# Kernel optimization log

Measured on AMD Instinct MI355X. Metric: run time of the kernel, lower is better.

Reference implementation:

```python
import jax, jax.numpy as jnp
import numpy as np

N_NODES = 20000
N_EDGES = 160000
N_GRAPHS = 100
IN_CH = 64
EDGE_DIM = 8
NEG_SLOPE = 0.2


def _gatv2(x, edge_index, edge_attr, Wl, Wr, We, att, b, heads, ch, n_nodes):
    # GATv2Conv: e_ij = att . leaky_relu(Wl x_j + Wr x_i [+ We e_ij]), softmax over dst i,
    # out_i = sum_j alpha_ij * (Wl x_j), concat heads, + bias.
    src, dst = edge_index[0], edge_index[1]
    xl = (x @ Wl).reshape(-1, heads, ch)  # [N,H,C] source-side transform
    xr = (x @ Wr).reshape(-1, heads, ch)  # [N,H,C] target-side transform
    m = xl[src] + xr[dst]                 # [E,H,C]
    if edge_attr is not None:
        m = m + (edge_attr @ We).reshape(-1, heads, ch)
    m = jax.nn.leaky_relu(m, NEG_SLOPE)
    logit = jnp.einsum('ehc,hc->eh', m, att)                     # [E,H]
    mx = jax.ops.segment_max(logit, dst, num_segments=n_nodes)   # [N,H]
    ex = jnp.exp(logit - mx[dst])
    den = jax.ops.segment_sum(ex, dst, num_segments=n_nodes)     # [N,H]
    alpha = ex / (den[dst] + 1e-16)                              # [E,H]
    out = jax.ops.segment_sum(alpha[:, :, None] * xl[src], dst, num_segments=n_nodes)
    return out.reshape(-1, heads * ch) + b


def setup_inputs() -> dict:
    key = jax.random.key(0)
    ks = jax.random.split(key, 24)
    def rn(k, shape, fan_in):
        return jax.random.normal(k, shape, dtype=jnp.float32) / np.sqrt(fan_in)
    inp = {}
    inp['x'] = jax.random.normal(ks[0], (N_NODES, IN_CH), dtype=jnp.float32)
    inp['edge_attr'] = jax.random.uniform(ks[1], (N_EDGES, EDGE_DIM), dtype=jnp.float32)
    inp['Wl1'] = rn(ks[2], (IN_CH, 1024), IN_CH)
    inp['Wr1'] = rn(ks[3], (IN_CH, 1024), IN_CH)
    inp['We1'] = rn(ks[4], (EDGE_DIM, 1024), EDGE_DIM)
    inp['att1'] = rn(ks[5], (4, 256), 256)
    inp['b1'] = jnp.zeros((1024,), jnp.float32)
    inp['Wl2'] = rn(ks[6], (1024, 256), 1024)
    inp['Wr2'] = rn(ks[7], (1024, 256), 1024)
    inp['We2'] = rn(ks[8], (EDGE_DIM, 256), EDGE_DIM)
    inp['att2'] = rn(ks[9], (4, 64), 64)
    inp['b2'] = jnp.zeros((256,), jnp.float32)
    inp['Wlp'] = rn(ks[10], (256, 384), 256)
    inp['Wrp'] = rn(ks[11], (256, 384), 256)
    inp['attp'] = rn(ks[12], (6, 64), 64)
    inp['bp'] = jnp.zeros((384,), jnp.float32)
    inp['Wfc1'] = rn(ks[13], (384, 64), 384)
    inp['bfc1'] = jnp.zeros((64,), jnp.float32)
    inp['Wfc2'] = rn(ks[14], (64, 1), 64)
    inp['bfc2'] = jnp.zeros((1,), jnp.float32)
    inp['edge_index'] = jax.random.randint(ks[15], (2, N_EDGES), 0, N_NODES, dtype=jnp.int32)
    inp['edge_index_master'] = jax.random.randint(ks[16], (2, N_EDGES), 0, N_NODES, dtype=jnp.int32)
    inp['n_nodes'] = jnp.full((N_GRAPHS,), N_NODES // N_GRAPHS, dtype=jnp.int32)
    return inp


def reference(x, edge_attr, Wl1, Wr1, We1, att1, b1, Wl2, Wr2, We2, att2, b2,
              Wlp, Wrp, attp, bp, Wfc1, bfc1, Wfc2, bfc2,
              edge_index, edge_index_master, n_nodes):
    h = _gatv2(x, edge_index, edge_attr, Wl1, Wr1, We1, att1, b1, 4, 256, N_NODES)
    h = jax.nn.relu(h)
    h = _gatv2(h, edge_index, edge_attr, Wl2, Wr2, We2, att2, b2, 4, 64, N_NODES)
    h = jax.nn.relu(h)
    h = _gatv2(h, edge_index_master, None, Wlp, Wrp, None, attp, bp, 6, 64, N_NODES)
    last_idx = jnp.cumsum(n_nodes) - 1          # master node = last node of each graph
    master = h[last_idx]                        # [G,384] (dropout p=0 -> identity)
    z = jax.nn.relu(master @ Wfc1 + bfc1)
    return z @ Wfc2 + bfc2                      # [G,1]
```

## Files before the change

### kernel.cpp

```cpp
#include <hip/hip_runtime.h>
#include <hip/hip_bf16.h>

#define DIV_UP(a,b) (((a)+(b)-1)/(b))

typedef __attribute__((ext_vector_type(8))) short short8;
typedef __attribute__((ext_vector_type(4))) float floatx4;
typedef _Float16 half2t __attribute__((ext_vector_type(2)));

static __device__ __forceinline__ unsigned short f2bf(float v) {
    unsigned u = __builtin_bit_cast(unsigned, v);
    u += 0x7fffu + ((u >> 16) & 1u);
    return (unsigned short)(u >> 16);
}
static __device__ __forceinline__ unsigned short f2h(float v) {
    _Float16 h = (_Float16)v;
    return __builtin_bit_cast(unsigned short, h);
}
static __device__ __forceinline__ float fexp2(float x) { return __builtin_amdgcn_exp2f(x); }

static __device__ __forceinline__ half2t mk_h2(float lo, float hi) {
    half2t h; h[0] = (_Float16)lo; h[1] = (_Float16)hi; return h;
}
static __device__ __forceinline__ unsigned ph2(float lo, float hi) {
    return __builtin_bit_cast(unsigned, mk_h2(lo, hi));
}
static __device__ __forceinline__ float fdot2h(half2t a, half2t b, float c) {
    return __builtin_amdgcn_fdot2(a, b, c, false);
}
static __device__ __forceinline__ unsigned uget(const uint4 v, int k) {
    return k == 0 ? v.x : k == 1 ? v.y : k == 2 ? v.z : v.w;
}
static __device__ __forceinline__ float h2lo(half2t h) { return (float)h[0]; }
static __device__ __forceinline__ float h2hi(half2t h) { return (float)h[1]; }

template <int CPL> struct RawT;
template <> struct RawT<8> { using T = uint4; };
template <> struct RawT<4> { using T = uint2; };
template <> struct RawT<2> { using T = unsigned; };

template <int CPL>
static __device__ __forceinline__ void loadh2(const unsigned short* p, half2t* d) {
    if constexpr (CPL == 8) {
        uint4 v = *(const uint4*)p;
        d[0] = __builtin_bit_cast(half2t, v.x);
        d[1] = __builtin_bit_cast(half2t, v.y);
        d[2] = __builtin_bit_cast(half2t, v.z);
        d[3] = __builtin_bit_cast(half2t, v.w);
    } else if constexpr (CPL == 4) {
        uint2 v = *(const uint2*)p;
        d[0] = __builtin_bit_cast(half2t, v.x);
        d[1] = __builtin_bit_cast(half2t, v.y);
    } else {
        unsigned v = *(const unsigned*)p;
        d[0] = __builtin_bit_cast(half2t, v);
    }
}

template <int CPL>
static __device__ __forceinline__ void store_bf16v(unsigned short* p, const float* s) {
    unsigned short tmp[CPL];
#pragma unroll
    for (int c = 0; c < CPL; ++c) tmp[c] = f2bf(s[c]);
    if constexpr (CPL == 8) *(uint4*)p = *(uint4*)tmp;
    else if constexpr (CPL == 4) *(ushort4*)p = *(ushort4*)tmp;
    else if constexpr (CPL == 2) *(ushort2*)p = *(ushort2*)tmp;
    else p[0] = tmp[0];
}

template <int CTRL>
static __device__ __forceinline__ float dpp_mv(float x) {
    int r = __builtin_amdgcn_update_dpp(0, __builtin_bit_cast(int, x), CTRL, 0xF, 0xF, false);
    return __builtin_bit_cast(float, r);
}
template <int G>
static __device__ __forceinline__ float group_reduce(float x) {
    x += dpp_mv<0xB1>(x);
    x += dpp_mv<0x4E>(x);
    x += dpp_mv<0x124>(x);
    x += dpp_mv<0x128>(x);
    if constexpr (G >= 32) x += __shfl_xor(x, 16, 64);
    if constexpr (G >= 64) x += __shfl_xor(x, 32, 64);
    return x;
}

static __device__ __forceinline__ void tr_pair(const float* Wa, const float* Wb, int K, int Nn,
                                               unsigned short* Wt, int i) {
    int tot = K * Nn;
    const float* W = (i < tot) ? Wa : Wb;
    unsigned short* dst = Wt + ((i < tot) ? 0 : (size_t)Nn * K);
    int ii = (i < tot) ? i : i - tot;
    int k = ii % K, n = ii / K;
    dst[(size_t)n * K + k] = f2bf(W[(size_t)k * Nn + n]);
}

__global__ void prep_all(const float* __restrict__ x,
                         const float* __restrict__ Wl1, const float* __restrict__ Wr1,
                         const float* __restrict__ Wl2, const float* __restrict__ Wr2,
                         const float* __restrict__ Wlp, const float* __restrict__ Wrp,
                         unsigned short* __restrict__ xbf,
                         unsigned short* __restrict__ wt1, unsigned short* __restrict__ wt2,
                         unsigned short* __restrict__ wt3, int N) {
    const int S1 = 2 * 64 * 1024, S2 = 2 * 1024 * 256, S3 = 2 * 256 * 384;
    int id = blockIdx.x * blockDim.x + threadIdx.x;
    if (id < S1) tr_pair(Wl1, Wr1, 64, 1024, wt1, id);
    else if (id < S1 + S2) tr_pair(Wl2, Wr2, 1024, 256, wt2, id - S1);
    else if (id < S1 + S2 + S3) tr_pair(Wlp, Wrp, 256, 384, wt3, id - S1 - S2);
    else {
        int i = id - S1 - S2 - S3;
        if (i < N * 64) xbf[i] = f2bf(x[i]);
    }
}

#define GLOAD_LDS16(gp, lp) \
    __builtin_amdgcn_global_load_lds((const __attribute__((address_space(1))) void*)(gp), \
                                     (__attribute__((address_space(3))) void*)(lp), 16, 0, 0)

__global__ __launch_bounds__(256) void gemm_mfma(
    const unsigned short* __restrict__ A, const unsigned short* __restrict__ Bt,
    unsigned short* __restrict__ CL, unsigned short* __restrict__ CR,
    int M, int NL, int K) {
    __shared__ unsigned short As[128 * 32];
    __shared__ unsigned short Bs[128 * 32];
    const int tid = threadIdx.x;
    const int m0 = blockIdx.y * 128, n0 = blockIdx.x * 128;
    const bool left = (n0 < NL);
    unsigned short* Cb = left ? CL : CR;
    const int nbase = left ? n0 : n0 - NL;
    const int wave = tid >> 6, lane = tid & 63;
    const int wm = (wave >> 1) * 64, wn = (wave & 1) * 64;
    const int r15 = lane & 15, quad = lane >> 4;
    const int srow = lane >> 2, scol = (lane & 3) * 8;
    const int arow0 = m0 + 32 * wave + srow;
    const int brow0 = n0 + 32 * wave + srow;
    const unsigned short* ap0 = A + (size_t)arow0 * K + scol;
    const unsigned short* ap1 = ap0 + (size_t)16 * K;
    const unsigned short* bp0 = Bt + (size_t)brow0 * K + scol;
    const unsigned short* bp1 = bp0 + (size_t)16 * K;
    unsigned short* alds0 = As + (32 * wave) * 32;
    unsigned short* alds1 = alds0 + 16 * 32;
    unsigned short* blds0 = Bs + (32 * wave) * 32;
    unsigned short* blds1 = blds0 + 16 * 32;
    const bool av0 = arow0 < M, av1 = (arow0 + 16) < M;
    floatx4 acc[4][4];
#pragma unroll
    for (int i = 0; i < 4; ++i)
#pragma unroll
        for (int j = 0; j < 4; ++j) acc[i][j] = (floatx4)0.f;

    for (int k0 = 0; k0 < K; k0 += 32) {
        if (av0) GLOAD_LDS16(ap0, alds0);
        if (av1) GLOAD_LDS16(ap1, alds1);
        GLOAD_LDS16(bp0, blds0);
        GLOAD_LDS16(bp1, blds1);
        ap0 += 32; ap1 += 32; bp0 += 32; bp1 += 32;
        __syncthreads();
        short8 af[4], bfr[4];
#pragma unroll
        for (int i = 0; i < 4; ++i)
            af[i] = *(const short8*)(&As[(wm + i * 16 + r15) * 32 + quad * 8]);
#pragma unroll
        for (int j = 0; j < 4; ++j)
            bfr[j] = *(const short8*)(&Bs[(wn + j * 16 + r15) * 32 + quad * 8]);
#pragma unroll
        for (int i = 0; i < 4; ++i)
#pragma unroll
            for (int j = 0; j < 4; ++j)
                acc[i][j] = __builtin_amdgcn_mfma_f32_16x16x32_bf16(af[i], bfr[j], acc[i][j], 0, 0, 0);
        __syncthreads();
    }
#pragma unroll
    for (int i = 0; i < 4; ++i)
#pragma unroll
        for (int j = 0; j < 4; ++j)
#pragma unroll
            for (int r = 0; r < 4; ++r) {
                int m = m0 + wm + i * 16 + quad * 4 + r;
                int n = nbase + wn + j * 16 + r15;
                if (m < M) Cb[(size_t)m * NL + n] = f2h(acc[i][j][r]);
            }
}

__global__ void count2_kernel(const int* __restrict__ dst0, const int* __restrict__ dst1,
                              int E, int N, int* __restrict__ cnt) {
    int e = blockIdx.x * blockDim.x + threadIdx.x;
    if (e < E) atomicAdd(&cnt[dst0[e]], 1);
    else if (e < 2 * E) atomicAdd(&cnt[N + dst1[e - E]], 1);
}

__global__ __launch_bounds__(1024) void scan_kernel(const int* __restrict__ cnt_all, int N,
                                                    int* __restrict__ off_all, int* __restrict__ cur_all) {
    const int* cnt = cnt_all + blockIdx.x * N;
    int* off = off_all + blockIdx.x * (N + 1);
    int* cur = cur_all + blockIdx.x * N;
    __shared__ int part[1024];
    int t = threadIdx.x;
    int per = (N + 1023) >> 10;
    int base = t * per;
    int s = 0;
    for (int i = 0; i < per; ++i) { int idx = base + i; if (idx < N) s += cnt[idx]; }
    part[t] = s;
    __syncthreads();
    for (int d2 = 1; d2 < 1024; d2 <<= 1) {
        int v = (t >= d2) ? part[t - d2] : 0;
        __syncthreads();
        part[t] += v;
        __syncthreads();
    }
    int pre = (t == 0) ? 0 : part[t - 1];
    for (int i = 0; i < per; ++i) {
        int idx = base + i;
        if (idx < N) { off[idx] = pre; cur[idx] = pre; pre += cnt[idx]; }
    }
    if (t == 1023) off[N] = part[1023];
}

__global__ void fill2_kernel(const int* __restrict__ src0, const int* __restrict__ dst0,
                             const int* __restrict__ src1, const int* __restrict__ dst1,
                             int E, int N, int* __restrict__ cur, int2* __restrict__ edges,
                             int* __restrict__ srcs) {
    int e = blockIdx.x * blockDim.x + threadIdx.x;
    if (e < E) {
        int p = atomicAdd(&cur[dst0[e]], 1);
        edges[p] = make_int2(src0[e], e);
        srcs[p] = src0[e];
    } else if (e < 2 * E) {
        int i = e - E;
        int p = atomicAdd(&cur[N + dst1[i]], 1);
        srcs[E + p] = src1[i];
    }
}

__global__ void ea_gather_kernel(const float* __restrict__ ea, const int2* __restrict__ edges,
                                 uint4* __restrict__ ead, int E) {
    int j = blockIdx.x * blockDim.x + threadIdx.x;
    if (j >= E) return;
    int ey = edges[j].y;
    const float4* s = (const float4*)(ea + (size_t)ey * 8);
    float4 a = s[0], b = s[1];
    uint4 o0, o1;
    o0.x = ph2(a.x, a.x); o0.y = ph2(a.y, a.y);
    o0.z = ph2(a.z, a.z); o0.w = ph2(a.w, a.w);
    o1.x = ph2(b.x, b.x); o1.y = ph2(b.y, b.y);
    o1.z = ph2(b.z, b.z); o1.w = ph2(b.w, b.w);
    ead[2 * j]     = o0;
    ead[2 * j + 1] = o1;
}

template <int D, int CPL, int G, int NE>
static __device__ __forceinline__ void hase_group(
    const unsigned short* __restrict__ xl, const uint4* __restrict__ ej,
    const int* __restrict__ sj, const unsigned* wbu,
    const half2t (&att2)[CPL / 2], const half2t (&xr2)[CPL / 2], int c0,
    float& m, float& l, float (&acc)[CPL]) {
    constexpr int P = CPL / 2;
    int src[NE];
#pragma unroll
    for (int n = 0; n < NE; ++n) src[n] = sj[n];
    uint4 ev0[NE], ev1[NE];
#pragma unroll
    for (int n = 0; n < NE; ++n) { ev0[n] = ej[2 * n]; ev1[n] = ej[2 * n + 1]; }
    half2t xv[NE][P], z[NE][P];
#pragma unroll
    for (int n = 0; n < NE; ++n) {
        loadh2<CPL>(xl + (size_t)src[n] * D + c0, xv[n]);
#pragma unroll
        for (int p = 0; p < P; ++p) z[n][p] = xv[n][p] + xr2[p];
    }
#pragma unroll
    for (int k = 0; k < 8; ++k) {
        half2t wk[P];
        if constexpr (CPL == 8) {
            uint4 w4 = *(const uint4*)(wbu + k * (D / 2));
            wk[0] = __builtin_bit_cast(half2t, w4.x);
            wk[1] = __builtin_bit_cast(half2t, w4.y);
            wk[2] = __builtin_bit_cast(half2t, w4.z);
            wk[3] = __builtin_bit_cast(half2t, w4.w);
        } else {
            uint2 w2 = *(const uint2*)(wbu + k * (D / 2));
            wk[0] = __builtin_bit_cast(half2t, w2.x);
            wk[1] = __builtin_bit_cast(half2t, w2.y);
        }
#pragma unroll
        for (int n = 0; n < NE; ++n) {
            unsigned eu = (k < 4) ? uget(ev0[n], k) : uget(ev1[n], k - 4);
            half2t e2 = __builtin_bit_cast(half2t, eu);
#pragma unroll
            for (int p = 0; p < P; ++p)
                z[n][p] = __builtin_elementwise_fma(e2, wk[p], z[n][p]);
        }
    }
    const half2t c02 = mk_h2(0.2f, 0.2f);
    float lg[NE];
#pragma unroll
    for (int n = 0; n < NE; ++n) {
        float t = 0.f;
#pragma unroll
        for (int p = 0; p < P; ++p) {
            half2t zz = z[n][p];
            half2t lz = __builtin_elementwise_max(zz, zz * c02);
            t = fdot2h(att2[p], lz, t);
        }
        lg[n] = group_reduce<G>(t);
    }
    float mn = m;
#pragma unroll
    for (int n = 0; n < NE; ++n) mn = fmaxf(mn, lg[n]);
    float sc = fexp2(m - mn);
    float pr[NE], ps = 0.f;
#pragma unroll
    for (int n = 0; n < NE; ++n) { pr[n] = fexp2(lg[n] - mn); ps += pr[n]; }
    m = mn;
    l = fmaf(l, sc, ps);
#pragma unroll
    for (int p = 0; p < P; ++p) {
        float t0 = pr[0] * h2lo(xv[0][p]);
        float t1 = pr[0] * h2hi(xv[0][p]);
#pragma unroll
        for (int n = 1; n < NE; ++n) {
            t0 = fmaf(pr[n], h2lo(xv[n][p]), t0);
            t1 = fmaf(pr[n], h2hi(xv[n][p]), t1);
        }
        acc[2 * p]     = fmaf(acc[2 * p],     sc, t0);
        acc[2 * p + 1] = fmaf(acc[2 * p + 1], sc, t1);
    }
}

template <int D, int C, int CB, int WPN, bool RELU>
__global__ __launch_bounds__(256) void attn_hase(
    const unsigned short* __restrict__ xl, const unsigned short* __restrict__ xr,
    const uint4* __restrict__ ead4,
    const float* __restrict__ We, const float* __restrict__ att,
    const int* __restrict__ srcs, const int* __restrict__ off,
    const float* __restrict__ bias, unsigned short* __restrict__ outp, int N) {
    constexpr int CPL = CB / 64;
    constexpr int P = CPL / 2;
    constexpr int HW = CB / C;
    constexpr int G = 64 / HW;
    constexpr int NPB = 4 / WPN;
    __shared__ unsigned wsh[4 * D];
    for (int idx = threadIdx.x; idx < 4 * D; idx += 256) {
        int k = idx / (D / 2);
        int r = idx - k * (D / 2);
        int c = 2 * r;
        wsh[idx] = ph2(We[(size_t)k * D + c], We[(size_t)k * D + c + 1]);
    }
    __syncthreads();

    const int wid = threadIdx.x >> 6, lane = threadIdx.x & 63;
    const int wv = wid % WPN, wn = wid / WPN;
    const int c0 = wv * CB + lane * CPL;
    const unsigned* wbu = wsh + wv * (CB / 2) + lane * (CPL / 2);

    const float L2E = 1.4426950408889634f;
    half2t att2[P];
#pragma unroll
    for (int p = 0; p < P; ++p)
        att2[p] = mk_h2(att[c0 + 2 * p] * L2E, att[c0 + 2 * p + 1] * L2E);

    for (int node = blockIdx.x * NPB + wn; node < N; node += gridDim.x * NPB) {
        half2t xr2[P];
        loadh2<CPL>(xr + (size_t)node * D + c0, xr2);
        float m = -1e30f, l = 0.f, acc[CPL];
#pragma unroll
        for (int c = 0; c < CPL; ++c) acc[c] = 0.f;

        const int jb = __builtin_amdgcn_readfirstlane(off[node]);
        const int je = __builtin_amdgcn_readfirstlane(off[node + 1]);
        int j = jb;
        for (; j + 4 <= je; j += 4)
            hase_group<D, CPL, G, 4>(xl, ead4 + 2 * j, srcs + j, wbu, att2, xr2, c0, m, l, acc);
        for (; j < je; ++j)
            hase_group<D, CPL, G, 1>(xl, ead4 + 2 * j, srcs + j, wbu, att2, xr2, c0, m, l, acc);

        float inv = 1.f / (l + 1e-16f);
        float r[CPL];
#pragma unroll
        for (int c = 0; c < CPL; ++c) {
            r[c] = fmaf(acc[c], inv, bias[c0 + c]);
            if constexpr (RELU) r[c] = fmaxf(r[c], 0.f);
        }
        store_bf16v<CPL>(outp + (size_t)node * D + c0, r);
    }
}

template <int D, int CPL, int G, int NE>
static __device__ __forceinline__ void noe_group(
    const unsigned short* __restrict__ xl, const int* __restrict__ sj,
    const half2t (&att2)[CPL / 2], const half2t (&xr2)[CPL / 2], int c0,
    float& m, float& l, float (&acc)[CPL]) {
    constexpr int P = CPL / 2;
    int src[NE];
#pragma unroll
    for (int n = 0; n < NE; ++n) src[n] = sj[n];
    half2t xv[NE][P];
#pragma unroll
    for (int n = 0; n < NE; ++n)
        loadh2<CPL>(xl + (size_t)src[n] * D + c0, xv[n]);
    const half2t c02 = mk_h2(0.2f, 0.2f);
    float lg[NE];
#pragma unroll
    for (int n = 0; n < NE; ++n) {
        float t = 0.f;
#pragma unroll
        for (int p = 0; p < P; ++p) {
            half2t zz = xv[n][p] + xr2[p];
            half2t lz = __builtin_elementwise_max(zz, zz * c02);
            t = fdot2h(att2[p], lz, t);
        }
        lg[n] = group_reduce<G>(t);
    }
    float mn = m;
#pragma unroll
    for (int n = 0; n < NE; ++n) mn = fmaxf(mn, lg[n]);
    float sc = fexp2(m - mn);
    float pr[NE], ps = 0.f;
#pragma unroll
    for (int n = 0; n < NE; ++n) { pr[n] = fexp2(lg[n] - mn); ps += pr[n]; }
    m = mn;
    l = fmaf(l, sc, ps);
#pragma unroll
    for (int p = 0; p < P; ++p) {
        float t0 = pr[0] * h2lo(xv[0][p]);
        float t1 = pr[0] * h2hi(xv[0][p]);
#pragma unroll
        for (int n = 1; n < NE; ++n) {
            t0 = fmaf(pr[n], h2lo(xv[n][p]), t0);
            t1 = fmaf(pr[n], h2hi(xv[n][p]), t1);
        }
        acc[2 * p]     = fmaf(acc[2 * p],     sc, t0);
        acc[2 * p + 1] = fmaf(acc[2 * p + 1], sc, t1);
    }
}

template <int D, int C, int CB, bool RELU>
static __device__ __forceinline__ void attn_wave3(
    const unsigned short* __restrict__ xl, const unsigned short* __restrict__ xr,
    const float* __restrict__ att,
    const int* __restrict__ srcs, int jb, int je,
    const float* __restrict__ bias, float* __restrict__ outp,
    int node, int cb, int lane) {
    constexpr int CPL = CB / 64;
    constexpr int P = CPL / 2;
    constexpr int HW = CB / C;
    constexpr int G = 64 / HW;
    const int c0 = cb + lane * CPL;
    const float L2E = 1.4426950408889634f;

    half2t xr2[P], att2[P];
    loadh2<CPL>(xr + (size_t)node * D + c0, xr2);
#pragma unroll
    for (int p = 0; p < P; ++p)
        att2[p] = mk_h2(att[c0 + 2 * p] * L2E, att[c0 + 2 * p + 1] * L2E);

    float m = -1e30f, l = 0.f, acc[CPL];
#pragma unroll
    for (int c = 0; c < CPL; ++c) acc[c] = 0.f;

    int j = jb;
    for (; j + 4 <= je; j += 4)
        noe_group<D, CPL, G, 4>(xl, srcs + j, att2, xr2, c0, m, l, acc);
    for (; j < je; ++j)
        noe_group<D, CPL, G, 1>(xl, srcs + j, att2, xr2, c0, m, l, acc);

    float inv = 1.f / (l + 1e-16f);
    float* out = outp + (size_t)node * D + c0;
    float tmp[CPL];
#pragma unroll
    for (int c = 0; c < CPL; ++c) {
        float r = fmaf(acc[c], inv, bias[c0 + c]);
        if constexpr (RELU) r = fmaxf(r, 0.f);
        tmp[c] = r;
    }
    if constexpr (CPL == 4) *(float4*)out = *(float4*)tmp;
    else if constexpr (CPL == 2) *(float2*)out = *(float2*)tmp;
    else out[0] = tmp[0];
}

template <int D, int C, int CB0, int CB1, bool RELU>
__global__ __launch_bounds__(256) void attn_noe(
    const unsigned short* __restrict__ xl, const unsigned short* __restrict__ xr,
    const float* __restrict__ att,
    const int* __restrict__ srcs, const int* __restrict__ off,
    const float* __restrict__ bias, float* __restrict__ outp, int N) {
    const int wid = threadIdx.x >> 6, lane = threadIdx.x & 63;
    const int gw = blockIdx.x * 4 + wid;
    const int node = gw >> 1, wv = gw & 1;
    if (node >= N) return;
    const int jb = __builtin_amdgcn_readfirstlane(off[node]);
    const int je = __builtin_amdgcn_readfirstlane(off[node + 1]);
    if (wv == 0)
        attn_wave3<D, C, CB0, RELU>(xl, xr, att, srcs, jb, je, bias, outp, node, 0, lane);
    else
        attn_wave3<D, C, CB1, RELU>(xl, xr, att, srcs, jb, je, bias, outp, node, CB0, lane);
}

__global__ void mlp_kernel(const float* __restrict__ h3, const int* __restrict__ nn,
                           const float* __restrict__ Wfc1, const float* __restrict__ bfc1,
                           const float* __restrict__ Wfc2, const float* __restrict__ bfc2,
                           float* __restrict__ out, int G) {
    int g = blockIdx.x, t = threadIdx.x;
    int s = 0;
    for (int k = 0; k <= g; ++k) s += nn[k];
    const float* row = h3 + (size_t)(s - 1) * 384;
    float z = bfc1[t];
    for (int k = 0; k < 384; ++k) z = fmaf(row[k], Wfc1[k * 64 + t], z);
    z = fmaxf(z, 0.f);
    float v = z * Wfc2[t];
#pragma unroll
    for (int o = 32; o; o >>= 1) v += __shfl_xor(v, o, 64);
    if (t == 0) out[g] = v + bfc2[0];
}

extern "C" void kernel_launch(void* const* d_in, const int* in_sizes, int n_in,
                              void* d_out, int out_size, void* d_ws, size_t ws_size,
                              hipStream_t stream) {
    const float* x    = (const float*)d_in[0];
    const float* ea   = (const float*)d_in[1];
    const float* Wl1  = (const float*)d_in[2];
    const float* Wr1  = (const float*)d_in[3];
    const float* We1  = (const float*)d_in[4];
    const float* att1 = (const float*)d_in[5];
    const float* b1   = (const float*)d_in[6];
    const float* Wl2  = (const float*)d_in[7];
    const float* Wr2  = (const float*)d_in[8];
    const float* We2  = (const float*)d_in[9];
    const float* att2 = (const float*)d_in[10];
    const float* b2   = (const float*)d_in[11];
    const float* Wlp  = (const float*)d_in[12];
    const float* Wrp  = (const float*)d_in[13];
    const float* attp = (const float*)d_in[14];
    const float* bp   = (const float*)d_in[15];
    const float* Wfc1 = (const float*)d_in[16];
    const float* bfc1 = (const float*)d_in[17];
    const float* Wfc2 = (const float*)d_in[18];
    const float* bfc2 = (const float*)d_in[19];
    const int* ei     = (const int*)d_in[20];
    const int* eim    = (const int*)d_in[21];
    const int* nn     = (const int*)d_in[22];

    const int N = in_sizes[0] / 64;
    const int E = in_sizes[20] / 2;
    const int G = in_sizes[22];
    const int* src1 = ei,  *dst1 = ei + E;
    const int* srcm = eim, *dstm = eim + E;

    char* w = (char*)d_ws;
    size_t o = 0;
    auto alloc = [&](size_t b) { size_t r = o; o += (b + 255) & ~(size_t)255; return r; };
    char* R1 = w + alloc((size_t)N * 2048 * 2);
    unsigned short* xl1 = (unsigned short*)R1;
    unsigned short* xr1 = xl1 + (size_t)N * 1024;
    unsigned short* xl3 = (unsigned short*)R1;
    unsigned short* xr3 = xl3 + (size_t)N * 384;
    float* h3 = (float*)(R1 + (size_t)N * 768 * 2 + 256);
    unsigned short* h1   = (unsigned short*)(w + alloc((size_t)N * 1024 * 2));
    char* R2 = w + alloc((size_t)N * 512 * 2);
    unsigned short* xl2 = (unsigned short*)R2;
    unsigned short* xr2 = xl2 + (size_t)N * 256;
    unsigned short* h2   = (unsigned short*)(w + alloc((size_t)N * 256 * 2));
    unsigned short* xbf  = (unsigned short*)(w + alloc((size_t)N * 64 * 2));
    unsigned short* wt1  = (unsigned short*)(w + alloc((size_t)2048 * 64 * 2));
    unsigned short* wt2  = (unsigned short*)(w + alloc((size_t)512 * 1024 * 2));
    unsigned short* wt3  = (unsigned short*)(w + alloc((size_t)768 * 256 * 2));
    int*  cnt   = (int*)(w + alloc((size_t)2 * N * 4));
    int*  off   = (int*)(w + alloc((size_t)2 * (N + 1) * 4));
    int*  cur   = (int*)(w + alloc((size_t)2 * N * 4));
    char* eReg  = w + alloc((size_t)2 * E * 8 + 4096);
    int2* edges = (int2*)eReg;
    int*  srcs  = (int*)(eReg + (size_t)E * 8);
    (void)ws_size; (void)n_in; (void)out_size;

    uint4* ead1 = (uint4*)R2;
    uint4* ead2 = (uint4*)h1;

    dim3 blk(256);

    {
        int tot = 2 * 64 * 1024 + 2 * 1024 * 256 + 2 * 256 * 384 + N * 64;
        prep_all<<<DIV_UP(tot, 256), blk, 0, stream>>>(x, Wl1, Wr1, Wl2, Wr2, Wlp, Wrp,
                                                       xbf, wt1, wt2, wt3, N);
    }

    hipMemsetAsync(cnt, 0, (size_t)2 * N * 4, stream);
    count2_kernel<<<DIV_UP(2 * E, 256), blk, 0, stream>>>(dst1, dstm, E, N, cnt);
    scan_kernel<<<2, 1024, 0, stream>>>(cnt, N, off, cur);
    fill2_kernel<<<DIV_UP(2 * E, 256), blk, 0, stream>>>(src1, dst1, srcm, dstm, E, N, cur,
                                                         edges, srcs);
    ea_gather_kernel<<<DIV_UP(E, 256), blk, 0, stream>>>(ea, edges, ead1, E);
    const int* off3 = off + (N + 1);
    const int* srcs3 = srcs + E;

    gemm_mfma<<<dim3(2048 / 128, DIV_UP(N, 128)), blk, 0, stream>>>(
        xbf, wt1, xl1, xr1, N, 1024, 64);
    attn_hase<1024, 256, 512, 2, true><<<2560, blk, 0, stream>>>(
        xl1, xr1, ead1, We1, att1, srcs, off, b1, h1, N);

    gemm_mfma<<<dim3(512 / 128, DIV_UP(N, 128)), blk, 0, stream>>>(
        h1, wt2, xl2, xr2, N, 256, 1024);
    ea_gather_kernel<<<DIV_UP(E, 256), blk, 0, stream>>>(ea, edges, ead2, E);
    attn_hase<256, 64, 256, 1, true><<<1280, blk, 0, stream>>>(
        xl2, xr2, ead2, We2, att2, srcs, off, b2, h2, N);

    gemm_mfma<<<dim3(768 / 128, DIV_UP(N, 128)), blk, 0, stream>>>(
        h2, wt3, xl3, xr3, N, 384, 256);
    attn_noe<384, 64, 256, 128, false><<<DIV_UP(N, 2), blk, 0, stream>>>(
        xl3, xr3, attp, srcs3, off3, bp, h3, N);

    mlp_kernel<<<G, 64, 0, stream>>>(h3, nn, Wfc1, bfc1, Wfc2, bfc2, (float*)d_out, G);
}
```

Before: 420.5 us.

## Split each node's edge list across two waves and merge softmax partials via LDS

The edge-attention kernel now assigns two waves per node feature slice. Each wave processes half of the node's incoming edges with an online softmax, and the partial max, sum and accumulators are merged through shared memory before the output is written. This doubles parallelism per node to hide gather latency on xl. In exchange it adds LDS traffic, two block-wide barriers per iteration, and fewer nodes per block.

```diff
diff --git a/kernel.cpp b/kernel.cpp
--- a/kernel.cpp
+++ b/kernel.cpp
@@ -336,8 +336,10 @@
     constexpr int P = CPL / 2;
     constexpr int HW = CB / C;
     constexpr int G = 64 / HW;
-    constexpr int NPB = 4 / WPN;
+    constexpr int NW = WPN * 2;
+    constexpr int NPB = 4 / NW;
     __shared__ unsigned wsh[4 * D];
+    __shared__ float cmb[NPB][WPN][64][CPL + 2];
     for (int idx = threadIdx.x; idx < 4 * D; idx += 256) {
         int k = idx / (D / 2);
         int r = idx - k * (D / 2);
@@ -347,7 +349,10 @@
     __syncthreads();
 
     const int wid = threadIdx.x >> 6, lane = threadIdx.x & 63;
-    const int wv = wid % WPN, wn = wid / WPN;
+    const int wn = wid / NW;
+    const int wr = wid - wn * NW;
+    const int wv = wr % WPN;
+    const int ep = wr / WPN;
     const int c0 = wv * CB + lane * CPL;
     const unsigned* wbu = wsh + wv * (CB / 2) + lane * (CPL / 2);
 
@@ -357,29 +362,51 @@
     for (int p = 0; p < P; ++p)
         att2[p] = mk_h2(att[c0 + 2 * p] * L2E, att[c0 + 2 * p + 1] * L2E);
 
-    for (int node = blockIdx.x * NPB + wn; node < N; node += gridDim.x * NPB) {
+    for (int base = blockIdx.x * NPB; base < N; base += gridDim.x * NPB) {
+        const int node = base + wn;
+        float m = -1e30f, l = 0.f, acc[CPL];
+#pragma unroll
+        for (int c = 0; c < CPL; ++c) acc[c] = 0.f;
         half2t xr2[P];
-        loadh2<CPL>(xr + (size_t)node * D + c0, xr2);
-        float m = -1e30f, l = 0.f, acc[CPL];
-#pragma unroll
-        for (int c = 0; c < CPL; ++c) acc[c] = 0.f;
-
-        const int jb = __builtin_amdgcn_readfirstlane(off[node]);
-        const int je = __builtin_amdgcn_readfirstlane(off[node + 1]);
-        int j = jb;
-        for (; j + 4 <= je; j += 4)
-            hase_group<D, CPL, G, 4>(xl, ead4 + 2 * j, srcs + j, wbu, att2, xr2, c0, m, l, acc);
-        for (; j < je; ++j)
-            hase_group<D, CPL, G, 1>(xl, ead4 + 2 * j, srcs + j, wbu, att2, xr2, c0, m, l, acc);
-
-        float inv = 1.f / (l + 1e-16f);
-        float r[CPL];
-#pragma unroll
-        for (int c = 0; c < CPL; ++c) {
-            r[c] = fmaf(acc[c], inv, bias[c0 + c]);
-            if constexpr (RELU) r[c] = fmaxf(r[c], 0.f);
-        }
-        store_bf16v<CPL>(outp + (size_t)node * D + c0, r);
+#pragma unroll
+        for (int p = 0; p < P; ++p) xr2[p] = mk_h2(0.f, 0.f);
+
+        if (node < N) {
+            loadh2<CPL>(xr + (size_t)node * D + c0, xr2);
+            const int jb = __builtin_amdgcn_readfirstlane(off[node]);
+            const int je = __builtin_amdgcn_readfirstlane(off[node + 1]);
+            const int half = (je - jb + 1) >> 1;
+            int j  = ep ? jb + half : jb;
+            const int j1 = ep ? je : jb + half;
+            for (; j + 4 <= j1; j += 4)
+                hase_group<D, CPL, G, 4>(xl, ead4 + 2 * j, srcs + j, wbu, att2, xr2, c0, m, l, acc);
+            for (; j < j1; ++j)
+                hase_group<D, CPL, G, 1>(xl, ead4 + 2 * j, srcs + j, wbu, att2, xr2, c0, m, l, acc);
+        }
+        if (ep == 1) {
+            cmb[wn][wv][lane][0] = m;
+            cmb[wn][wv][lane][1] = l;
+#pragma unroll
+            for (int c = 0; c < CPL; ++c) cmb[wn][wv][lane][2 + c] = acc[c];
+        }
+        __syncthreads();
+        if (ep == 0 && node < N) {
+            float m1 = cmb[wn][wv][lane][0];
+            float l1 = cmb[wn][wv][lane][1];
+            float mn = fmaxf(m, m1);
+            float s0 = fexp2(m - mn), s1 = fexp2(m1 - mn);
+            float lt = fmaf(l, s0, l1 * s1);
+            float inv = 1.f / (lt + 1e-16f);
+            float r[CPL];
+#pragma unroll
+            for (int c = 0; c < CPL; ++c) {
+                float a = fmaf(acc[c], s0, cmb[wn][wv][lane][2 + c] * s1);
+                r[c] = fmaf(a, inv, bias[c0 + c]);
+                if constexpr (RELU) r[c] = fmaxf(r[c], 0.f);
+            }
+            store_bf16v<CPL>(outp + (size_t)node * D + c0, r);
+        }
+        __syncthreads();
     }
 }
 
```

Measured after the change: 452.2 us. 1.08x slower.
